# Optimization experiments

Measured on AMD Instinct MI355X. Metric: run time of the kernel, lower is better.

## Reference

```python
import jax, jax.numpy as jnp
import numpy as np

QMIN = 0.1
EPS = 1e-7
NN, NP_, NE = 200_000, 5_000, 10_000_000


def setup_inputs() -> dict:
    key = jax.random.key(0)
    ks = jax.random.split(key, 8)
    beta = jax.random.uniform(ks[0], (NN,), jnp.float32)
    x = jax.random.normal(ks[1], (NN, 3), jnp.float32)
    isTrack = jax.random.randint(ks[2], (NN,), 0, 2, jnp.int32)
    pt = jax.random.randint(ks[3], (NN,), 0, NP_, jnp.int32)
    noise = jax.random.uniform(ks[4], (NN,)) < 0.1
    parent_target = jnp.where(noise, -1, pt).astype(jnp.int32)
    particle_idx = jnp.arange(NP_, dtype=jnp.int32)
    particle_class = jax.random.randint(ks[5], (NP_,), 0, 5, jnp.int32)
    edge_node = jax.random.randint(ks[6], (NE,), 0, NN, jnp.int32)
    edge_particle = jax.random.randint(ks[7], (NE,), 0, NP_, jnp.int32)
    return {"beta": beta, "x": x, "isTrack": isTrack, "parent_target": parent_target,
            "particle_idx": particle_idx, "particle_class": particle_class,
            "edge_node": edge_node, "edge_particle": edge_particle}


def reference(beta, x, isTrack, parent_target, particle_idx, particle_class, edge_node, edge_particle):
    E = edge_node.shape[0]
    Nn = beta.shape[0]
    Np = particle_idx.shape[0]
    f32 = beta.dtype

    # edge label: node's parent target == particle's idx (ApplyTo*EdgeLabel)
    label = (parent_target[edge_node] == particle_idx[edge_particle]).astype(f32)

    # condensation charge q = arctanh(clamped beta)^2 + qmin
    cb = jnp.clip(beta, EPS, 1.0 - EPS)
    q = jnp.arctanh(cb) ** 2 + QMIN

    # ---- ChildToParent mailbox (masked gathers on edges) ----
    betas = beta[edge_node] * label                              # [E]
    track_m = isTrack[edge_node].astype(f32) * label             # [E]
    pclass_m = particle_class[edge_particle].astype(f32) * label  # [E]
    # where(parent_class < 2, betas, isTrack*betas)
    beta_mail = jnp.where(pclass_m < 2.0, betas, track_m * betas)

    # ---- per-particle max-beta reduction with argmax payload selection ----
    # init 'max beta'/'max q'/'max x' are zeros, concatenated first in the torch code
    max_beta = jax.ops.segment_max(beta_mail, edge_particle, num_segments=Np)
    max_beta = jnp.maximum(max_beta, 0.0)
    hit = (beta_mail == max_beta[edge_particle]) & (max_beta[edge_particle] > 0.0)
    winner = jnp.where(hit, jnp.arange(E, dtype=jnp.int32), -1)
    best_edge = jax.ops.segment_max(winner, edge_particle, num_segments=Np)
    valid = best_edge >= 0
    safe = jnp.maximum(best_edge, 0)
    qs = q[edge_node] * label
    xs = x[edge_node] * label[:, None]
    max_q = jnp.where(valid, qs[safe], 0.0)            # [Np]
    max_x = jnp.where(valid[:, None], xs[safe], 0.0)   # [Np,3]

    # ---- ParentToChild potentials (ParentToChildEF) ----
    diff = max_x[edge_particle] - x[edge_node]          # [E,3]
    dist = jnp.sqrt(jnp.sum(diff * diff, axis=1))       # [E]
    mq = max_q[edge_particle]
    v_attract = 3.0 * label * mq * dist * dist
    v_repulse = (1.0 - label) * jnp.maximum(2.0 - dist, 0.0) * mq

    # ---- sum mailbox to nodes (ParentToChildNF) ----
    attract = jax.ops.segment_sum(v_attract, edge_node, num_segments=Nn)
    repulse = jax.ops.segment_sum(v_repulse, edge_node, num_segments=Nn)
    node_lv = q * (attract + repulse)                   # [Nn]
    return node_lv
```

## Files before the change

kernel.cpp:

```cpp
#include <hip/hip_runtime.h>

#define QMIN_V 0.1f
#define EPS_V  1e-7f


__global__ void init_ws_kernel(unsigned long long* __restrict__ packed,
                               float* __restrict__ accum, int np, int nn) {
    int tid = blockIdx.x * blockDim.x + threadIdx.x;
    int stride = gridDim.x * blockDim.x;
    for (int j = tid; j < np; j += stride) packed[j] = 0ULL;
    for (int j = tid; j < nn; j += stride) accum[j] = 0.0f;
}

__global__ void prep_xpt_kernel(const float* __restrict__ x,
                                const int* __restrict__ pt,
                                float4* __restrict__ xpt, int nn) {
    int i = blockIdx.x * blockDim.x + threadIdx.x;
    if (i >= nn) return;
    xpt[i] = make_float4(x[3 * i + 0], x[3 * i + 1], x[3 * i + 2],
                         __int_as_float(pt[i]));
}

__global__ void passA_kernel(const int* __restrict__ edge_node,
                             const int* __restrict__ edge_particle,
                             const float* __restrict__ beta,
                             const int* __restrict__ isTrack,
                             const int* __restrict__ pt,
                             const int* __restrict__ pidx,
                             const int* __restrict__ pclass,
                             unsigned long long* __restrict__ packed,
                             int np, int ne8, int ne) {
    extern __shared__ int s_pidx[];
    for (int j = threadIdx.x; j < np; j += blockDim.x) s_pidx[j] = pidx[j];
    __syncthreads();

    int tid = blockIdx.x * blockDim.x + threadIdx.x;
    int stride = gridDim.x * blockDim.x;
    const int4* en4 = reinterpret_cast<const int4*>(edge_node);
    const int4* ep4 = reinterpret_cast<const int4*>(edge_particle);

    for (int i = tid; i < ne8; i += stride) {
        int4 a0 = en4[2 * i], a1 = en4[2 * i + 1];
        int4 b0 = ep4[2 * i], b1 = ep4[2 * i + 1];
        int n[8] = {a0.x, a0.y, a0.z, a0.w, a1.x, a1.y, a1.z, a1.w};
        int p[8] = {b0.x, b0.y, b0.z, b0.w, b1.x, b1.y, b1.z, b1.w};
        int t[8];
#pragma unroll
        for (int k = 0; k < 8; ++k) t[k] = pt[n[k]];
        int q[8];
#pragma unroll
        for (int k = 0; k < 8; ++k) q[k] = s_pidx[p[k]];
#pragma unroll
        for (int k = 0; k < 8; ++k) {
            if (t[k] == q[k]) {
                float b = beta[n[k]];
                int pc = pclass[p[k]];
                float bm = (pc < 2) ? b : b * (float)isTrack[n[k]];
                if (bm > 0.0f) {
                    unsigned long long key =
                        ((unsigned long long)__float_as_uint(bm) << 32) |
                        (unsigned int)(8 * i + k);
                    atomicMax(&packed[p[k]], key);
                }
            }
        }
    }
    for (int e = ne8 * 8 + tid; e < ne; e += stride) {
        int n = edge_node[e];
        int p = edge_particle[e];
        if (pt[n] == pidx[p]) {
            float b = beta[n];
            int pc = pclass[p];
            float bm = (pc < 2) ? b : b * (float)isTrack[n];
            if (bm > 0.0f) {
                unsigned long long key =
                    ((unsigned long long)__float_as_uint(bm) << 32) |
                    (unsigned int)e;
                atomicMax(&packed[p], key);
            }
        }
    }
}

__global__ void passP_kernel(const unsigned long long* __restrict__ packed,
                             const int* __restrict__ edge_node,
                             const float* __restrict__ beta,
                             const float* __restrict__ x,
                             const int* __restrict__ pidx,
                             float4* __restrict__ maxdata,
                             float* __restrict__ mq, int np) {
    int p = blockIdx.x * blockDim.x + threadIdx.x;
    if (p >= np) return;
    unsigned long long key = packed[p];
    unsigned int bm_bits = (unsigned int)(key >> 32);
    float mqv = 0.0f, mx = 0.0f, my = 0.0f, mz = 0.0f;
    if (bm_bits != 0u) {
        int e = (int)(key & 0xffffffffULL);
        int n = edge_node[e];
        float b = beta[n];
        float cb = fminf(fmaxf(b, EPS_V), 1.0f - EPS_V);
        float a = atanhf(cb);
        mqv = a * a + QMIN_V;
        mx = x[3 * n + 0];
        my = x[3 * n + 1];
        mz = x[3 * n + 2];
    }
    maxdata[p] = make_float4(mx, my, mz, __int_as_float(pidx[p]));
    mq[p] = mqv;
}

template <int USE_XPT>
__global__ void passB_kernel(const int* __restrict__ edge_node,
                             const int* __restrict__ edge_particle,
                             const float* __restrict__ x,
                             const int* __restrict__ pt,
                             const float4* __restrict__ xpt,
                             const float4* __restrict__ maxdata,
                             const float* __restrict__ mq,
                             float* __restrict__ accum,
                             int np, int ne4, int ne) {
    extern __shared__ float s_mq[];
    for (int j = threadIdx.x; j < np; j += blockDim.x) s_mq[j] = mq[j];
    __syncthreads();

    int tid = blockIdx.x * blockDim.x + threadIdx.x;
    int stride = gridDim.x * blockDim.x;
    const int4* en4 = reinterpret_cast<const int4*>(edge_node);
    const int4* ep4 = reinterpret_cast<const int4*>(edge_particle);

    for (int i = tid; i < ne4; i += stride) {
        int4 a = en4[i];
        int4 b = ep4[i];
        int n[4] = {a.x, a.y, a.z, a.w};
        int p[4] = {b.x, b.y, b.z, b.w};
        float m[4];
#pragma unroll
        for (int k = 0; k < 4; ++k) m[k] = s_mq[p[k]];
        float4 md[4];
        float xv0[4], xv1[4], xv2[4];
        int ptv[4];
#pragma unroll
        for (int k = 0; k < 4; ++k) {
            if (m[k] > 0.0f) {
                md[k] = maxdata[p[k]];
                if (USE_XPT) {
                    float4 xp = xpt[n[k]];
                    xv0[k] = xp.x; xv1[k] = xp.y; xv2[k] = xp.z;
                    ptv[k] = __float_as_int(xp.w);
                } else {
                    xv0[k] = x[3 * n[k] + 0];
                    xv1[k] = x[3 * n[k] + 1];
                    xv2[k] = x[3 * n[k] + 2];
                    ptv[k] = pt[n[k]];
                }
            }
        }
#pragma unroll
        for (int k = 0; k < 4; ++k) {
            if (m[k] > 0.0f) {
                float dx = md[k].x - xv0[k];
                float dy = md[k].y - xv1[k];
                float dz = md[k].z - xv2[k];
                float d2 = dx * dx + dy * dy + dz * dz;
                bool label = (ptv[k] == __float_as_int(md[k].w));
                float v;
                if (label) v = 3.0f * m[k] * d2;
                else       v = fmaxf(2.0f - sqrtf(d2), 0.0f) * m[k];
                if (v != 0.0f) atomicAdd(&accum[n[k]], v);
            }
        }
    }
    for (int e = ne4 * 4 + tid; e < ne; e += stride) {
        int n = edge_node[e];
        int p = edge_particle[e];
        float m = s_mq[p];
        if (m > 0.0f) {
            float4 md = maxdata[p];
            float x0, x1, x2; int ptv;
            if (USE_XPT) {
                float4 xp = xpt[n];
                x0 = xp.x; x1 = xp.y; x2 = xp.z; ptv = __float_as_int(xp.w);
            } else {
                x0 = x[3 * n + 0]; x1 = x[3 * n + 1]; x2 = x[3 * n + 2];
                ptv = pt[n];
            }
            float dx = md.x - x0, dy = md.y - x1, dz = md.z - x2;
            float d2 = dx * dx + dy * dy + dz * dz;
            bool label = (ptv == __float_as_int(md.w));
            float v = label ? (3.0f * m * d2)
                            : (fmaxf(2.0f - sqrtf(d2), 0.0f) * m);
            if (v != 0.0f) atomicAdd(&accum[n], v);
        }
    }
}

__global__ void passN_kernel(const float* __restrict__ beta,
                             const float* __restrict__ accum,
                             float* __restrict__ out, int nn) {
    int i = blockIdx.x * blockDim.x + threadIdx.x;
    if (i >= nn) return;
    float b = beta[i];
    float cb = fminf(fmaxf(b, EPS_V), 1.0f - EPS_V);
    float a = atanhf(cb);
    out[i] = (a * a + QMIN_V) * accum[i];
}

extern "C" void kernel_launch(void* const* d_in, const int* in_sizes, int n_in,
                              void* d_out, int out_size, void* d_ws, size_t ws_size,
                              hipStream_t stream) {
    const float* beta    = (const float*)d_in[0];
    const float* x       = (const float*)d_in[1];
    const int*   isTrack = (const int*)d_in[2];
    const int*   pt      = (const int*)d_in[3];
    const int*   pidx    = (const int*)d_in[4];
    const int*   pclass  = (const int*)d_in[5];
    const int*   en      = (const int*)d_in[6];
    const int*   ep      = (const int*)d_in[7];
    float* out = (float*)d_out;

    int nn = in_sizes[0];
    int np = in_sizes[4];
    int ne = in_sizes[6];

    char* ws = (char*)d_ws;
    size_t off = 0;
    float4* maxdata = (float4*)(ws + off); off += (size_t)np * 16;
    size_t xpt_off = off;
    size_t need_xpt = off + (size_t)nn * 16 + (size_t)np * 8 + (size_t)np * 4
                      + (size_t)nn * 4;
    bool use_xpt = (ws_size >= need_xpt);
    float4* xpt = nullptr;
    if (use_xpt) { xpt = (float4*)(ws + xpt_off); off += (size_t)nn * 16; }
    unsigned long long* packed = (unsigned long long*)(ws + off); off += (size_t)np * 8;
    float* mq = (float*)(ws + off); off += (size_t)np * 4;
    float* accum = (float*)(ws + off);

    int ne8 = ne / 8;
    int ne4 = ne / 4;
    int lds_bytes = np * (int)sizeof(int);

    init_ws_kernel<<<256, 256, 0, stream>>>(packed, accum, np, nn);
    if (use_xpt)
        prep_xpt_kernel<<<(nn + 255) / 256, 256, 0, stream>>>(x, pt, xpt, nn);
    passA_kernel<<<2048, 256, lds_bytes, stream>>>(en, ep, beta, isTrack, pt,
                                                   pidx, pclass, packed,
                                                   np, ne8, ne);
    passP_kernel<<<(np + 255) / 256, 256, 0, stream>>>(packed, en, beta, x,
                                                       pidx, maxdata, mq, np);
    if (use_xpt)
        passB_kernel<1><<<2048, 256, lds_bytes, stream>>>(en, ep, x, pt, xpt,
                                                          maxdata, mq, accum,
                                                          np, ne4, ne);
    else
        passB_kernel<0><<<2048, 256, lds_bytes, stream>>>(en, ep, x, pt, xpt,
                                                          maxdata, mq, accum,
                                                          np, ne4, ne);
    passN_kernel<<<(nn + 255) / 256, 256, 0, stream>>>(beta, accum, out, nn);
}
```

Measured before the change: 233.5 us.

## Software-pipeline edge passes with prefetched indices and fused prep/init kernel

The two edge-streaming passes now use a two-stage software pipeline: edge index vectors are loaded two iterations ahead with nontemporal loads, and the dependent gathers run one iteration ahead, to hide gather latency. The max-q value is packed into the w lane of the per-particle float4 and pidx moves to LDS. As a result, pass B gathers unconditionally instead of branching on mq>0. The init and xpt-prep kernels are merged into one launch, and launch bounds are added. The risks are higher register pressure and extra gathers for edges whose particle has zero mq.

```diff
diff --git a/kernel.cpp b/kernel.cpp
--- a/kernel.cpp
+++ b/kernel.cpp
@@ -3,71 +3,103 @@
 #define QMIN_V 0.1f
 #define EPS_V  1e-7f
 
-
-__global__ void init_ws_kernel(unsigned long long* __restrict__ packed,
-                               float* __restrict__ accum, int np, int nn) {
-    int tid = blockIdx.x * blockDim.x + threadIdx.x;
-    int stride = gridDim.x * blockDim.x;
-    for (int j = tid; j < np; j += stride) packed[j] = 0ULL;
-    for (int j = tid; j < nn; j += stride) accum[j] = 0.0f;
-}
-
-__global__ void prep_xpt_kernel(const float* __restrict__ x,
-                                const int* __restrict__ pt,
-                                float4* __restrict__ xpt, int nn) {
+typedef int iv4 __attribute__((ext_vector_type(4)));
+typedef float fv4 __attribute__((ext_vector_type(4)));
+
+
+template <int USE_XPT>
+__global__ void prep_kernel(const float* __restrict__ x,
+                            const int* __restrict__ pt,
+                            float4* __restrict__ xpt,
+                            unsigned long long* __restrict__ packed,
+                            float* __restrict__ accum, int np, int nn) {
     int i = blockIdx.x * blockDim.x + threadIdx.x;
-    if (i >= nn) return;
-    xpt[i] = make_float4(x[3 * i + 0], x[3 * i + 1], x[3 * i + 2],
-                         __int_as_float(pt[i]));
-}
-
-__global__ void passA_kernel(const int* __restrict__ edge_node,
-                             const int* __restrict__ edge_particle,
-                             const float* __restrict__ beta,
-                             const int* __restrict__ isTrack,
-                             const int* __restrict__ pt,
-                             const int* __restrict__ pidx,
-                             const int* __restrict__ pclass,
-                             unsigned long long* __restrict__ packed,
-                             int np, int ne8, int ne) {
+    if (i < np) packed[i] = 0ULL;
+    if (i < nn) {
+        accum[i] = 0.0f;
+        if (USE_XPT)
+            xpt[i] = make_float4(x[3 * i + 0], x[3 * i + 1], x[3 * i + 2],
+                                 __int_as_float(pt[i]));
+    }
+}
+
+__global__ __launch_bounds__(256, 3)
+void passA_kernel(const int* __restrict__ en, const int* __restrict__ ep,
+                  const float* __restrict__ beta,
+                  const int* __restrict__ isTrack,
+                  const int* __restrict__ pt,
+                  const int* __restrict__ pidx,
+                  const int* __restrict__ pclass,
+                  unsigned long long* __restrict__ packed,
+                  int np, int ne8, int ne) {
     extern __shared__ int s_pidx[];
     for (int j = threadIdx.x; j < np; j += blockDim.x) s_pidx[j] = pidx[j];
     __syncthreads();
 
-    int tid = blockIdx.x * blockDim.x + threadIdx.x;
-    int stride = gridDim.x * blockDim.x;
-    const int4* en4 = reinterpret_cast<const int4*>(edge_node);
-    const int4* ep4 = reinterpret_cast<const int4*>(edge_particle);
-
-    for (int i = tid; i < ne8; i += stride) {
-        int4 a0 = en4[2 * i], a1 = en4[2 * i + 1];
-        int4 b0 = ep4[2 * i], b1 = ep4[2 * i + 1];
-        int n[8] = {a0.x, a0.y, a0.z, a0.w, a1.x, a1.y, a1.z, a1.w};
-        int p[8] = {b0.x, b0.y, b0.z, b0.w, b1.x, b1.y, b1.z, b1.w};
-        int t[8];
-#pragma unroll
-        for (int k = 0; k < 8; ++k) t[k] = pt[n[k]];
-        int q[8];
-#pragma unroll
-        for (int k = 0; k < 8; ++k) q[k] = s_pidx[p[k]];
-#pragma unroll
-        for (int k = 0; k < 8; ++k) {
-            if (t[k] == q[k]) {
-                float b = beta[n[k]];
-                int pc = pclass[p[k]];
-                float bm = (pc < 2) ? b : b * (float)isTrack[n[k]];
-                if (bm > 0.0f) {
-                    unsigned long long key =
-                        ((unsigned long long)__float_as_uint(bm) << 32) |
-                        (unsigned int)(8 * i + k);
-                    atomicMax(&packed[p[k]], key);
+    const int tid = blockIdx.x * blockDim.x + threadIdx.x;
+    const int stride = gridDim.x * blockDim.x;
+    const iv4* en4 = reinterpret_cast<const iv4*>(en);
+    const iv4* ep4 = reinterpret_cast<const iv4*>(ep);
+
+    if (tid < ne8) {
+        int iB = (tid + stride < ne8) ? (tid + stride) : tid;
+        iv4 eA0 = __builtin_nontemporal_load(&en4[2 * tid]);
+        iv4 eA1 = __builtin_nontemporal_load(&en4[2 * tid + 1]);
+        iv4 pA0 = __builtin_nontemporal_load(&ep4[2 * tid]);
+        iv4 pA1 = __builtin_nontemporal_load(&ep4[2 * tid + 1]);
+        iv4 eB0 = __builtin_nontemporal_load(&en4[2 * iB]);
+        iv4 eB1 = __builtin_nontemporal_load(&en4[2 * iB + 1]);
+        iv4 pB0 = __builtin_nontemporal_load(&ep4[2 * iB]);
+        iv4 pB1 = __builtin_nontemporal_load(&ep4[2 * iB + 1]);
+
+        int nA[8], piA[8], tA[8], qA[8];
+#pragma unroll
+        for (int k = 0; k < 4; ++k) { nA[k] = eA0[k]; nA[k + 4] = eA1[k];
+                                      piA[k] = pA0[k]; piA[k + 4] = pA1[k]; }
+#pragma unroll
+        for (int k = 0; k < 8; ++k) tA[k] = pt[nA[k]];
+#pragma unroll
+        for (int k = 0; k < 8; ++k) qA[k] = s_pidx[piA[k]];
+
+        for (int i = tid; i < ne8; i += stride) {
+            int iC = (i + 2 * stride < ne8) ? (i + 2 * stride) : tid;
+            iv4 eC0 = __builtin_nontemporal_load(&en4[2 * iC]);
+            iv4 eC1 = __builtin_nontemporal_load(&en4[2 * iC + 1]);
+            iv4 pC0 = __builtin_nontemporal_load(&ep4[2 * iC]);
+            iv4 pC1 = __builtin_nontemporal_load(&ep4[2 * iC + 1]);
+
+            int nB[8], piB[8], tB[8], qB[8];
+#pragma unroll
+            for (int k = 0; k < 4; ++k) { nB[k] = eB0[k]; nB[k + 4] = eB1[k];
+                                          piB[k] = pB0[k]; piB[k + 4] = pB1[k]; }
+#pragma unroll
+            for (int k = 0; k < 8; ++k) tB[k] = pt[nB[k]];
+#pragma unroll
+            for (int k = 0; k < 8; ++k) qB[k] = s_pidx[piB[k]];
+
+#pragma unroll
+            for (int k = 0; k < 8; ++k) {
+                if (tA[k] == qA[k]) {
+                    float b = beta[nA[k]];
+                    int pc = pclass[piA[k]];
+                    float bm = (pc < 2) ? b : b * (float)isTrack[nA[k]];
+                    if (bm > 0.0f) {
+                        unsigned long long key =
+                            ((unsigned long long)__float_as_uint(bm) << 32) |
+                            (unsigned int)(8 * i + k);
+                        atomicMax(&packed[piA[k]], key);
+                    }
                 }
             }
+            eB0 = eC0; eB1 = eC1; pB0 = pC0; pB1 = pC1;
+#pragma unroll
+            for (int k = 0; k < 8; ++k) { nA[k] = nB[k]; piA[k] = piB[k];
+                                          tA[k] = tB[k]; qA[k] = qB[k]; }
         }
     }
     for (int e = ne8 * 8 + tid; e < ne; e += stride) {
-        int n = edge_node[e];
-        int p = edge_particle[e];
+        int n = en[e];
+        int p = ep[e];
         if (pt[n] == pidx[p]) {
             float b = beta[n];
             int pc = pclass[p];
@@ -83,114 +115,123 @@
 }
 
 __global__ void passP_kernel(const unsigned long long* __restrict__ packed,
-                             const int* __restrict__ edge_node,
+                             const int* __restrict__ en,
                              const float* __restrict__ beta,
                              const float* __restrict__ x,
-                             const int* __restrict__ pidx,
-                             float4* __restrict__ maxdata,
-                             float* __restrict__ mq, int np) {
+                             float4* __restrict__ mdq, int np) {
     int p = blockIdx.x * blockDim.x + threadIdx.x;
     if (p >= np) return;
     unsigned long long key = packed[p];
     unsigned int bm_bits = (unsigned int)(key >> 32);
-    float mqv = 0.0f, mx = 0.0f, my = 0.0f, mz = 0.0f;
+    float4 md = make_float4(0.0f, 0.0f, 0.0f, 0.0f);
     if (bm_bits != 0u) {
         int e = (int)(key & 0xffffffffULL);
-        int n = edge_node[e];
+        int n = en[e];
         float b = beta[n];
         float cb = fminf(fmaxf(b, EPS_V), 1.0f - EPS_V);
         float a = atanhf(cb);
-        mqv = a * a + QMIN_V;
-        mx = x[3 * n + 0];
-        my = x[3 * n + 1];
-        mz = x[3 * n + 2];
-    }
-    maxdata[p] = make_float4(mx, my, mz, __int_as_float(pidx[p]));
-    mq[p] = mqv;
+        md.x = x[3 * n + 0];
+        md.y = x[3 * n + 1];
+        md.z = x[3 * n + 2];
+        md.w = a * a + QMIN_V;
+    }
+    mdq[p] = md;
 }
 
 template <int USE_XPT>
-__global__ void passB_kernel(const int* __restrict__ edge_node,
-                             const int* __restrict__ edge_particle,
-                             const float* __restrict__ x,
-                             const int* __restrict__ pt,
-                             const float4* __restrict__ xpt,
-                             const float4* __restrict__ maxdata,
-                             const float* __restrict__ mq,
-                             float* __restrict__ accum,
-                             int np, int ne4, int ne) {
-    extern __shared__ float s_mq[];
-    for (int j = threadIdx.x; j < np; j += blockDim.x) s_mq[j] = mq[j];
+__global__ __launch_bounds__(256, 3)
+void passB_kernel(const int* __restrict__ en, const int* __restrict__ ep,
+                  const float* __restrict__ x, const int* __restrict__ pt,
+                  const float4* __restrict__ xpt,
+                  const float4* __restrict__ mdq,
+                  const int* __restrict__ pidx,
+                  float* __restrict__ accum,
+                  int np, int ne4, int ne) {
+    extern __shared__ int s_pidx[];
+    for (int j = threadIdx.x; j < np; j += blockDim.x) s_pidx[j] = pidx[j];
     __syncthreads();
 
-    int tid = blockIdx.x * blockDim.x + threadIdx.x;
-    int stride = gridDim.x * blockDim.x;
-    const int4* en4 = reinterpret_cast<const int4*>(edge_node);
-    const int4* ep4 = reinterpret_cast<const int4*>(edge_particle);
-
-    for (int i = tid; i < ne4; i += stride) {
-        int4 a = en4[i];
-        int4 b = ep4[i];
-        int n[4] = {a.x, a.y, a.z, a.w};
-        int p[4] = {b.x, b.y, b.z, b.w};
-        float m[4];
-#pragma unroll
-        for (int k = 0; k < 4; ++k) m[k] = s_mq[p[k]];
-        float4 md[4];
-        float xv0[4], xv1[4], xv2[4];
-        int ptv[4];
+    const int tid = blockIdx.x * blockDim.x + threadIdx.x;
+    const int stride = gridDim.x * blockDim.x;
+    const iv4* en4 = reinterpret_cast<const iv4*>(en);
+    const iv4* ep4 = reinterpret_cast<const iv4*>(ep);
+
+    if (tid < ne4) {
+        int iB = (tid + stride < ne4) ? (tid + stride) : tid;
+        iv4 eA = __builtin_nontemporal_load(&en4[tid]);
+        iv4 pA = __builtin_nontemporal_load(&ep4[tid]);
+        iv4 eB = __builtin_nontemporal_load(&en4[iB]);
+        iv4 pB = __builtin_nontemporal_load(&ep4[iB]);
+
+        float4 mA[4], xA[4];
+        int qA[4];
+#pragma unroll
+        for (int k = 0; k < 4; ++k) mA[k] = mdq[pA[k]];
 #pragma unroll
         for (int k = 0; k < 4; ++k) {
-            if (m[k] > 0.0f) {
-                md[k] = maxdata[p[k]];
-                if (USE_XPT) {
-                    float4 xp = xpt[n[k]];
-                    xv0[k] = xp.x; xv1[k] = xp.y; xv2[k] = xp.z;
-                    ptv[k] = __float_as_int(xp.w);
-                } else {
-                    xv0[k] = x[3 * n[k] + 0];
-                    xv1[k] = x[3 * n[k] + 1];
-                    xv2[k] = x[3 * n[k] + 2];
-                    ptv[k] = pt[n[k]];
-                }
+            int n = eA[k];
+            if (USE_XPT) xA[k] = xpt[n];
+            else xA[k] = make_float4(x[3 * n], x[3 * n + 1], x[3 * n + 2],
+                                     __int_as_float(pt[n]));
+        }
+#pragma unroll
+        for (int k = 0; k < 4; ++k) qA[k] = s_pidx[pA[k]];
+
+        for (int i = tid; i < ne4; i += stride) {
+            int iC = (i + 2 * stride < ne4) ? (i + 2 * stride) : tid;
+            iv4 eC = __builtin_nontemporal_load(&en4[iC]);
+            iv4 pC = __builtin_nontemporal_load(&ep4[iC]);
+
+            float4 mB[4], xB[4];
+            int qB[4];
+#pragma unroll
+            for (int k = 0; k < 4; ++k) mB[k] = mdq[pB[k]];
+#pragma unroll
+            for (int k = 0; k < 4; ++k) {
+                int n = eB[k];
+                if (USE_XPT) xB[k] = xpt[n];
+                else xB[k] = make_float4(x[3 * n], x[3 * n + 1], x[3 * n + 2],
+                                         __int_as_float(pt[n]));
             }
-        }
-#pragma unroll
-        for (int k = 0; k < 4; ++k) {
-            if (m[k] > 0.0f) {
-                float dx = md[k].x - xv0[k];
-                float dy = md[k].y - xv1[k];
-                float dz = md[k].z - xv2[k];
+#pragma unroll
+            for (int k = 0; k < 4; ++k) qB[k] = s_pidx[pB[k]];
+
+#pragma unroll
+            for (int k = 0; k < 4; ++k) {
+                float mq = mA[k].w;
+                float dx = mA[k].x - xA[k].x;
+                float dy = mA[k].y - xA[k].y;
+                float dz = mA[k].z - xA[k].z;
                 float d2 = dx * dx + dy * dy + dz * dz;
-                bool label = (ptv[k] == __float_as_int(md[k].w));
-                float v;
-                if (label) v = 3.0f * m[k] * d2;
-                else       v = fmaxf(2.0f - sqrtf(d2), 0.0f) * m[k];
-                if (v != 0.0f) atomicAdd(&accum[n[k]], v);
+                float dist = sqrtf(d2);
+                bool label = (__float_as_int(xA[k].w) == qA[k]);
+                float v = label ? (3.0f * mq * d2)
+                                : (fmaxf(2.0f - dist, 0.0f) * mq);
+                if (v > 0.0f) atomicAdd(&accum[eA[k]], v);
             }
+            eA = eB; pA = pB; eB = eC; pB = pC;
+#pragma unroll
+            for (int k = 0; k < 4; ++k) { mA[k] = mB[k]; xA[k] = xB[k]; qA[k] = qB[k]; }
         }
     }
     for (int e = ne4 * 4 + tid; e < ne; e += stride) {
-        int n = edge_node[e];
-        int p = edge_particle[e];
-        float m = s_mq[p];
-        if (m > 0.0f) {
-            float4 md = maxdata[p];
-            float x0, x1, x2; int ptv;
-            if (USE_XPT) {
-                float4 xp = xpt[n];
-                x0 = xp.x; x1 = xp.y; x2 = xp.z; ptv = __float_as_int(xp.w);
-            } else {
-                x0 = x[3 * n + 0]; x1 = x[3 * n + 1]; x2 = x[3 * n + 2];
-                ptv = pt[n];
-            }
-            float dx = md.x - x0, dy = md.y - x1, dz = md.z - x2;
-            float d2 = dx * dx + dy * dy + dz * dz;
-            bool label = (ptv == __float_as_int(md.w));
-            float v = label ? (3.0f * m * d2)
-                            : (fmaxf(2.0f - sqrtf(d2), 0.0f) * m);
-            if (v != 0.0f) atomicAdd(&accum[n], v);
-        }
+        int n = en[e];
+        int p = ep[e];
+        float4 md = mdq[p];
+        float mq = md.w;
+        float x0, x1, x2; int ptv;
+        if (USE_XPT) {
+            float4 xp = xpt[n];
+            x0 = xp.x; x1 = xp.y; x2 = xp.z; ptv = __float_as_int(xp.w);
+        } else {
+            x0 = x[3 * n]; x1 = x[3 * n + 1]; x2 = x[3 * n + 2]; ptv = pt[n];
+        }
+        float dx = md.x - x0, dy = md.y - x1, dz = md.z - x2;
+        float d2 = dx * dx + dy * dy + dz * dz;
+        bool label = (ptv == pidx[p]);
+        float v = label ? (3.0f * mq * d2)
+                        : (fmaxf(2.0f - sqrtf(d2), 0.0f) * mq);
+        if (v > 0.0f) atomicAdd(&accum[n], v);
     }
 }
 
@@ -224,36 +265,38 @@
 
     char* ws = (char*)d_ws;
     size_t off = 0;
-    float4* maxdata = (float4*)(ws + off); off += (size_t)np * 16;
+    float4* mdq = (float4*)(ws + off); off += (size_t)np * 16;
     size_t xpt_off = off;
-    size_t need_xpt = off + (size_t)nn * 16 + (size_t)np * 8 + (size_t)np * 4
-                      + (size_t)nn * 4;
+    size_t need_xpt = off + (size_t)nn * 16 + (size_t)np * 8 + (size_t)nn * 4;
     bool use_xpt = (ws_size >= need_xpt);
     float4* xpt = nullptr;
     if (use_xpt) { xpt = (float4*)(ws + xpt_off); off += (size_t)nn * 16; }
     unsigned long long* packed = (unsigned long long*)(ws + off); off += (size_t)np * 8;
-    float* mq = (float*)(ws + off); off += (size_t)np * 4;
     float* accum = (float*)(ws + off);
 
     int ne8 = ne / 8;
     int ne4 = ne / 4;
     int lds_bytes = np * (int)sizeof(int);
-
-    init_ws_kernel<<<256, 256, 0, stream>>>(packed, accum, np, nn);
+    int prep_blocks = ((nn > np ? nn : np) + 255) / 256;
+
     if (use_xpt)
-        prep_xpt_kernel<<<(nn + 255) / 256, 256, 0, stream>>>(x, pt, xpt, nn);
+        prep_kernel<1><<<prep_blocks, 256, 0, stream>>>(x, pt, xpt, packed,
+                                                        accum, np, nn);
+    else
+        prep_kernel<0><<<prep_blocks, 256, 0, stream>>>(x, pt, xpt, packed,
+                                                        accum, np, nn);
     passA_kernel<<<2048, 256, lds_bytes, stream>>>(en, ep, beta, isTrack, pt,
                                                    pidx, pclass, packed,
                                                    np, ne8, ne);
     passP_kernel<<<(np + 255) / 256, 256, 0, stream>>>(packed, en, beta, x,
-                                                       pidx, maxdata, mq, np);
+                                                       mdq, np);
     if (use_xpt)
         passB_kernel<1><<<2048, 256, lds_bytes, stream>>>(en, ep, x, pt, xpt,
-                                                          maxdata, mq, accum,
+                                                          mdq, pidx, accum,
                                                           np, ne4, ne);
     else
         passB_kernel<0><<<2048, 256, lds_bytes, stream>>>(en, ep, x, pt, xpt,
-                                                          maxdata, mq, accum,
+                                                          mdq, pidx, accum,
                                                           np, ne4, ne);
     passN_kernel<<<(nn + 255) / 256, 256, 0, stream>>>(beta, accum, out, nn);
 }
```

Result: slower. 334.9 us (+43.4%).

## Fuse init into prep kernel, use one-shot grids and nontemporal edge loads

Applied to the files above, without the earlier changes.

Merges the workspace zeroing and the xpt packing into a single prep kernel, removing one launch. Pass A and pass B now use one-shot grids sized to the edge count instead of 2048-block grid-stride loops. The edge index streams are read with nontemporal loads so they do not evict the cache lines holding gathered node data. The trade-off is many more blocks, each of which reloads the particle table into LDS, which adds shared-memory fill overhead.

```diff
diff --git a/kernel.cpp b/kernel.cpp
--- a/kernel.cpp
+++ b/kernel.cpp
@@ -3,51 +3,54 @@
 #define QMIN_V 0.1f
 #define EPS_V  1e-7f
 
-
-__global__ void init_ws_kernel(unsigned long long* __restrict__ packed,
-                               float* __restrict__ accum, int np, int nn) {
-    int tid = blockIdx.x * blockDim.x + threadIdx.x;
-    int stride = gridDim.x * blockDim.x;
-    for (int j = tid; j < np; j += stride) packed[j] = 0ULL;
-    for (int j = tid; j < nn; j += stride) accum[j] = 0.0f;
-}
-
-__global__ void prep_xpt_kernel(const float* __restrict__ x,
-                                const int* __restrict__ pt,
-                                float4* __restrict__ xpt, int nn) {
+typedef int iv4 __attribute__((ext_vector_type(4)));
+
+
+template <int USE_XPT>
+__global__ void prep_kernel(const float* __restrict__ x,
+                            const int* __restrict__ pt,
+                            float4* __restrict__ xpt,
+                            unsigned long long* __restrict__ packed,
+                            float* __restrict__ accum, int np, int nn) {
     int i = blockIdx.x * blockDim.x + threadIdx.x;
-    if (i >= nn) return;
-    xpt[i] = make_float4(x[3 * i + 0], x[3 * i + 1], x[3 * i + 2],
-                         __int_as_float(pt[i]));
-}
-
-__global__ void passA_kernel(const int* __restrict__ edge_node,
-                             const int* __restrict__ edge_particle,
+    if (i < np) packed[i] = 0ULL;
+    if (i < nn) {
+        accum[i] = 0.0f;
+        if (USE_XPT)
+            xpt[i] = make_float4(x[3 * i + 0], x[3 * i + 1], x[3 * i + 2],
+                                 __int_as_float(pt[i]));
+    }
+}
+
+__global__ void passA_kernel(const int* __restrict__ en, const int* __restrict__ ep,
                              const float* __restrict__ beta,
                              const int* __restrict__ isTrack,
                              const int* __restrict__ pt,
                              const int* __restrict__ pidx,
                              const int* __restrict__ pclass,
                              unsigned long long* __restrict__ packed,
-                             int np, int ne8, int ne) {
+                             int np, int ne) {
     extern __shared__ int s_pidx[];
     for (int j = threadIdx.x; j < np; j += blockDim.x) s_pidx[j] = pidx[j];
     __syncthreads();
 
     int tid = blockIdx.x * blockDim.x + threadIdx.x;
-    int stride = gridDim.x * blockDim.x;
-    const int4* en4 = reinterpret_cast<const int4*>(edge_node);
-    const int4* ep4 = reinterpret_cast<const int4*>(edge_particle);
-
-    for (int i = tid; i < ne8; i += stride) {
-        int4 a0 = en4[2 * i], a1 = en4[2 * i + 1];
-        int4 b0 = ep4[2 * i], b1 = ep4[2 * i + 1];
-        int n[8] = {a0.x, a0.y, a0.z, a0.w, a1.x, a1.y, a1.z, a1.w};
-        int p[8] = {b0.x, b0.y, b0.z, b0.w, b1.x, b1.y, b1.z, b1.w};
-        int t[8];
+    int base = tid * 8;
+    if (base >= ne) return;
+
+    if (base + 8 <= ne) {
+        const iv4* en4 = reinterpret_cast<const iv4*>(en);
+        const iv4* ep4 = reinterpret_cast<const iv4*>(ep);
+        iv4 e0 = __builtin_nontemporal_load(&en4[2 * tid]);
+        iv4 e1 = __builtin_nontemporal_load(&en4[2 * tid + 1]);
+        iv4 p0 = __builtin_nontemporal_load(&ep4[2 * tid]);
+        iv4 p1 = __builtin_nontemporal_load(&ep4[2 * tid + 1]);
+        int n[8], p[8], t[8], q[8];
+#pragma unroll
+        for (int k = 0; k < 4; ++k) { n[k] = e0[k]; n[k + 4] = e1[k];
+                                      p[k] = p0[k]; p[k + 4] = p1[k]; }
 #pragma unroll
         for (int k = 0; k < 8; ++k) t[k] = pt[n[k]];
-        int q[8];
 #pragma unroll
         for (int k = 0; k < 8; ++k) q[k] = s_pidx[p[k]];
 #pragma unroll
@@ -59,31 +62,32 @@
                 if (bm > 0.0f) {
                     unsigned long long key =
                         ((unsigned long long)__float_as_uint(bm) << 32) |
-                        (unsigned int)(8 * i + k);
+                        (unsigned int)(base + k);
                     atomicMax(&packed[p[k]], key);
                 }
             }
         }
-    }
-    for (int e = ne8 * 8 + tid; e < ne; e += stride) {
-        int n = edge_node[e];
-        int p = edge_particle[e];
-        if (pt[n] == pidx[p]) {
-            float b = beta[n];
-            int pc = pclass[p];
-            float bm = (pc < 2) ? b : b * (float)isTrack[n];
-            if (bm > 0.0f) {
-                unsigned long long key =
-                    ((unsigned long long)__float_as_uint(bm) << 32) |
-                    (unsigned int)e;
-                atomicMax(&packed[p], key);
+    } else {
+        for (int e = base; e < ne; ++e) {
+            int n = en[e];
+            int p = ep[e];
+            if (pt[n] == s_pidx[p]) {
+                float b = beta[n];
+                int pc = pclass[p];
+                float bm = (pc < 2) ? b : b * (float)isTrack[n];
+                if (bm > 0.0f) {
+                    unsigned long long key =
+                        ((unsigned long long)__float_as_uint(bm) << 32) |
+                        (unsigned int)e;
+                    atomicMax(&packed[p], key);
+                }
             }
         }
     }
 }
 
 __global__ void passP_kernel(const unsigned long long* __restrict__ packed,
-                             const int* __restrict__ edge_node,
+                             const int* __restrict__ en,
                              const float* __restrict__ beta,
                              const float* __restrict__ x,
                              const int* __restrict__ pidx,
@@ -96,7 +100,7 @@
     float mqv = 0.0f, mx = 0.0f, my = 0.0f, mz = 0.0f;
     if (bm_bits != 0u) {
         int e = (int)(key & 0xffffffffULL);
-        int n = edge_node[e];
+        int n = en[e];
         float b = beta[n];
         float cb = fminf(fmaxf(b, EPS_V), 1.0f - EPS_V);
         float a = atanhf(cb);
@@ -110,86 +114,77 @@
 }
 
 template <int USE_XPT>
-__global__ void passB_kernel(const int* __restrict__ edge_node,
-                             const int* __restrict__ edge_particle,
-                             const float* __restrict__ x,
-                             const int* __restrict__ pt,
+__global__ void passB_kernel(const int* __restrict__ en, const int* __restrict__ ep,
+                             const float* __restrict__ x, const int* __restrict__ pt,
                              const float4* __restrict__ xpt,
                              const float4* __restrict__ maxdata,
                              const float* __restrict__ mq,
                              float* __restrict__ accum,
-                             int np, int ne4, int ne) {
+                             int np, int ne) {
     extern __shared__ float s_mq[];
     for (int j = threadIdx.x; j < np; j += blockDim.x) s_mq[j] = mq[j];
     __syncthreads();
 
     int tid = blockIdx.x * blockDim.x + threadIdx.x;
-    int stride = gridDim.x * blockDim.x;
-    const int4* en4 = reinterpret_cast<const int4*>(edge_node);
-    const int4* ep4 = reinterpret_cast<const int4*>(edge_particle);
-
-    for (int i = tid; i < ne4; i += stride) {
-        int4 a = en4[i];
-        int4 b = ep4[i];
-        int n[4] = {a.x, a.y, a.z, a.w};
-        int p[4] = {b.x, b.y, b.z, b.w};
+    int base = tid * 4;
+    if (base >= ne) return;
+
+    if (base + 4 <= ne) {
+        const iv4* en4 = reinterpret_cast<const iv4*>(en);
+        const iv4* ep4 = reinterpret_cast<const iv4*>(ep);
+        iv4 e = __builtin_nontemporal_load(&en4[tid]);
+        iv4 p = __builtin_nontemporal_load(&ep4[tid]);
         float m[4];
 #pragma unroll
         for (int k = 0; k < 4; ++k) m[k] = s_mq[p[k]];
-        float4 md[4];
-        float xv0[4], xv1[4], xv2[4];
-        int ptv[4];
+        float4 md[4], xv[4];
 #pragma unroll
         for (int k = 0; k < 4; ++k) {
             if (m[k] > 0.0f) {
                 md[k] = maxdata[p[k]];
-                if (USE_XPT) {
-                    float4 xp = xpt[n[k]];
-                    xv0[k] = xp.x; xv1[k] = xp.y; xv2[k] = xp.z;
-                    ptv[k] = __float_as_int(xp.w);
-                } else {
-                    xv0[k] = x[3 * n[k] + 0];
-                    xv1[k] = x[3 * n[k] + 1];
-                    xv2[k] = x[3 * n[k] + 2];
-                    ptv[k] = pt[n[k]];
+                if (USE_XPT) xv[k] = xpt[e[k]];
+                else {
+                    int n = e[k];
+                    xv[k] = make_float4(x[3 * n], x[3 * n + 1], x[3 * n + 2],
+                                        __int_as_float(pt[n]));
                 }
             }
         }
 #pragma unroll
         for (int k = 0; k < 4; ++k) {
             if (m[k] > 0.0f) {
-                float dx = md[k].x - xv0[k];
-                float dy = md[k].y - xv1[k];
-                float dz = md[k].z - xv2[k];
+                float dx = md[k].x - xv[k].x;
+                float dy = md[k].y - xv[k].y;
+                float dz = md[k].z - xv[k].z;
                 float d2 = dx * dx + dy * dy + dz * dz;
-                bool label = (ptv[k] == __float_as_int(md[k].w));
-                float v;
-                if (label) v = 3.0f * m[k] * d2;
-                else       v = fmaxf(2.0f - sqrtf(d2), 0.0f) * m[k];
-                if (v != 0.0f) atomicAdd(&accum[n[k]], v);
-            }
-        }
-    }
-    for (int e = ne4 * 4 + tid; e < ne; e += stride) {
-        int n = edge_node[e];
-        int p = edge_particle[e];
-        float m = s_mq[p];
-        if (m > 0.0f) {
-            float4 md = maxdata[p];
-            float x0, x1, x2; int ptv;
-            if (USE_XPT) {
-                float4 xp = xpt[n];
-                x0 = xp.x; x1 = xp.y; x2 = xp.z; ptv = __float_as_int(xp.w);
-            } else {
-                x0 = x[3 * n + 0]; x1 = x[3 * n + 1]; x2 = x[3 * n + 2];
-                ptv = pt[n];
-            }
-            float dx = md.x - x0, dy = md.y - x1, dz = md.z - x2;
-            float d2 = dx * dx + dy * dy + dz * dz;
-            bool label = (ptv == __float_as_int(md.w));
-            float v = label ? (3.0f * m * d2)
-                            : (fmaxf(2.0f - sqrtf(d2), 0.0f) * m);
-            if (v != 0.0f) atomicAdd(&accum[n], v);
+                bool label = (__float_as_int(xv[k].w) == __float_as_int(md[k].w));
+                float v = label ? (3.0f * m[k] * d2)
+                                : (fmaxf(2.0f - sqrtf(d2), 0.0f) * m[k]);
+                if (v > 0.0f) atomicAdd(&accum[e[k]], v);
+            }
+        }
+    } else {
+        for (int e = base; e < ne; ++e) {
+            int n = en[e];
+            int p = ep[e];
+            float m = s_mq[p];
+            if (m > 0.0f) {
+                float4 md = maxdata[p];
+                float x0, x1, x2; int ptv;
+                if (USE_XPT) {
+                    float4 xp = xpt[n];
+                    x0 = xp.x; x1 = xp.y; x2 = xp.z; ptv = __float_as_int(xp.w);
+                } else {
+                    x0 = x[3 * n]; x1 = x[3 * n + 1]; x2 = x[3 * n + 2];
+                    ptv = pt[n];
+                }
+                float dx = md.x - x0, dy = md.y - x1, dz = md.z - x2;
+                float d2 = dx * dx + dy * dy + dz * dz;
+                bool label = (ptv == __float_as_int(md.w));
+                float v = label ? (3.0f * m * d2)
+                                : (fmaxf(2.0f - sqrtf(d2), 0.0f) * m);
+                if (v > 0.0f) atomicAdd(&accum[n], v);
+            }
         }
     }
 }
@@ -235,25 +230,31 @@
     float* mq = (float*)(ws + off); off += (size_t)np * 4;
     float* accum = (float*)(ws + off);
 
-    int ne8 = ne / 8;
-    int ne4 = ne / 4;
     int lds_bytes = np * (int)sizeof(int);
-
-    init_ws_kernel<<<256, 256, 0, stream>>>(packed, accum, np, nn);
+    int prep_blocks = ((nn > np ? nn : np) + 255) / 256;
+
+    int thrA = (ne + 7) / 8;
+    int blkA = (thrA + 255) / 256;
+    int thrB = (ne + 3) / 4;
+    int blkB = (thrB + 255) / 256;
+
     if (use_xpt)
-        prep_xpt_kernel<<<(nn + 255) / 256, 256, 0, stream>>>(x, pt, xpt, nn);
-    passA_kernel<<<2048, 256, lds_bytes, stream>>>(en, ep, beta, isTrack, pt,
-                                                   pidx, pclass, packed,
-                                                   np, ne8, ne);
+        prep_kernel<1><<<prep_blocks, 256, 0, stream>>>(x, pt, xpt, packed,
+                                                        accum, np, nn);
+    else
+        prep_kernel<0><<<prep_blocks, 256, 0, stream>>>(x, pt, xpt, packed,
+                                                        accum, np, nn);
+    passA_kernel<<<blkA, 256, lds_bytes, stream>>>(en, ep, beta, isTrack, pt,
+                                                   pidx, pclass, packed, np, ne);
     passP_kernel<<<(np + 255) / 256, 256, 0, stream>>>(packed, en, beta, x,
                                                        pidx, maxdata, mq, np);
     if (use_xpt)
-        passB_kernel<1><<<2048, 256, lds_bytes, stream>>>(en, ep, x, pt, xpt,
+        passB_kernel<1><<<blkB, 256, lds_bytes, stream>>>(en, ep, x, pt, xpt,
                                                           maxdata, mq, accum,
-                                                          np, ne4, ne);
+                                                          np, ne);
     else
-        passB_kernel<0><<<2048, 256, lds_bytes, stream>>>(en, ep, x, pt, xpt,
+        passB_kernel<0><<<blkB, 256, lds_bytes, stream>>>(en, ep, x, pt, xpt,
                                                           maxdata, mq, accum,
-                                                          np, ne4, ne);
+                                                          np, ne);
     passN_kernel<<<(nn + 255) / 256, 256, 0, stream>>>(beta, accum, out, nn);
 }
```

Result: slower. 256.5 us (+9.8%).
